# Kernel optimization log

Hardware: AMD Instinct MI355X
Metric: run time of the kernel (lower is better)

## Reference

```python
import jax, jax.numpy as jnp
import numpy as np

K = 16  # number of neighbors (module init arg)

def setup_inputs() -> dict:
    key = jax.random.key(0)
    M, D, N = 65536, 16, 64
    x = jax.random.normal(key, (M, D), dtype=jnp.float32)
    # equal-length segments: each point set has M // N points
    segs = jnp.full((N,), M // N, dtype=jnp.int64)
    return {"x": x, "segs": segs}

def reference(x, segs):
    # Segmented kNN graph. Segments are equal-length (static shapes for jit),
    # so the per-segment pairwise distance + top-k becomes a batched op.
    B = segs.shape[0]
    M, D = x.shape
    L = M // B  # points per segment
    pts = x.reshape(B, L, D)
    # squared euclidean distances within each segment: (B, L, L)
    sq = jnp.sum(pts * pts, axis=-1)
    d2 = sq[:, :, None] + sq[:, None, :] - 2.0 * jnp.einsum('bld,bmd->blm', pts, pts)
    # k smallest distances per point (includes self, as in DGL's knn_graph)
    _, idx = jax.lax.top_k(-d2, K)  # idx: (B, L, K), local indices within segment
    offsets = (jnp.arange(B, dtype=idx.dtype) * L)[:, None, None]
    src = (idx + offsets).reshape(-1)                      # neighbor -> global node id
    dst = (jnp.arange(L, dtype=idx.dtype)[None, :, None] + offsets)  # (B, L, 1)
    dst = jnp.broadcast_to(dst, (B, L, K)).reshape(-1)
    # edges point from k-nearest neighbors (predecessors) to each node
    return src, dst
```

## Files before the change

### kernel.cpp

```cpp
#include <hip/hip_runtime.h>
#include <stdint.h>


#define L_SEG 1024
#define M_PTS 65536

typedef __fp16 fp16x2 __attribute__((ext_vector_type(2)));
typedef __fp16 fp16x4 __attribute__((ext_vector_type(4)));
typedef float  f32x4  __attribute__((ext_vector_type(4)));

__device__ __forceinline__ uint32_t umn(uint32_t a, uint32_t b) { return a < b ? a : b; }
__device__ __forceinline__ uint32_t umx(uint32_t a, uint32_t b) { return a > b ? a : b; }

#define CE(arr, i, p) { uint32_t lo = umn(arr[i], arr[p]); uint32_t hi = umx(arr[i], arr[p]); arr[i] = lo; arr[p] = hi; }

__device__ __forceinline__ void clean16(uint32_t* A) {
    #pragma unroll
    for (int j = 8; j > 0; j >>= 1) {
        #pragma unroll
        for (int i = 0; i < 16; ++i) {
            int p = i ^ j;
            if (p > i) CE(A, i, p);
        }
    }
}

__device__ __forceinline__ void sort16(uint32_t* B) {
    #pragma unroll
    for (int p = 1; p < 16; p <<= 1) {
        #pragma unroll
        for (int k = p; k >= 1; k >>= 1) {
            #pragma unroll
            for (int j = (k & (p - 1)); j + k < 16; j += 2 * k) {
                #pragma unroll
                for (int i = 0; i <= ((k - 1 < 15 - j - k) ? k - 1 : 15 - j - k); ++i) {
                    if ((i + j) / (2 * p) == (i + j + k) / (2 * p)) CE(B, i + j, i + j + k);
                }
            }
        }
    }
}

__device__ __forceinline__ void keep16(uint32_t* A, const uint32_t* S) {
    #pragma unroll
    for (int i = 0; i < 16; ++i) A[i] = umn(A[i], S[15 - i]);
    clean16(A);
}

__device__ __forceinline__ void mergeg(uint32_t* A) {
    #pragma unroll
    for (int m = 16; m <= 32; m <<= 1) {
        uint32_t P[16];
        #pragma unroll
        for (int i = 0; i < 16; ++i) P[i] = (uint32_t)__shfl_xor((int)A[15 - i], m, 64);
        #pragma unroll
        for (int i = 0; i < 16; ++i) A[i] = umn(A[i], P[i]);
        clean16(A);
    }
}

__device__ __forceinline__ uint32_t sel4(const uint32_t* A, int g, int v) {
    uint32_t t01 = (g & 1) ? A[4 + v]  : A[v];
    uint32_t t23 = (g & 1) ? A[12 + v] : A[8 + v];
    return (g & 2) ? t23 : t01;
}

__global__ __launch_bounds__(256, 4) void knn_v9_kernel(const float* __restrict__ x,
                                                        int* __restrict__ out) {
    __shared__ __attribute__((aligned(16))) __fp16 sc[L_SEG * 16];
    __shared__ __attribute__((aligned(16))) float  ssq[L_SEG];
    __shared__ __attribute__((aligned(16))) __fp16 sq16[64 * 16];

    const int tid = threadIdx.x;
    const int b   = blockIdx.x;
    const int seg = (b & 7) * 8 + (b >> 7);
    const int qp  = (b >> 3) & 15;
    const float* xseg = x + (size_t)seg * (L_SEG * 16);
    const f32x4* gx4  = (const f32x4*)xseg;

    {
        fp16x4* scv = (fp16x4*)sc;
        #pragma unroll
        for (int i = 0; i < 16; ++i) {
            f32x4 v = gx4[tid + 256 * i];
            union { fp16x2 h2[2]; fp16x4 h4; } u;
            u.h2[0] = __builtin_amdgcn_cvt_pkrtz(-2.0f * v[0], -2.0f * v[1]);
            u.h2[1] = __builtin_amdgcn_cvt_pkrtz(-2.0f * v[2], -2.0f * v[3]);
            scv[tid + 256 * i] = u.h4;
        }
    }
    {
        const int c0 = tid << 2;
        #pragma unroll
        for (int c = 0; c < 4; ++c) {
            float s = 128.0f;
            #pragma unroll
            for (int d = 0; d < 4; ++d) {
                f32x4 v = gx4[(c0 + c) * 4 + d];
                s = __builtin_fmaf(v[0], v[0], s);
                s = __builtin_fmaf(v[1], v[1], s);
                s = __builtin_fmaf(v[2], v[2], s);
                s = __builtin_fmaf(v[3], v[3], s);
            }
            ssq[c0 + c] = s;
        }
    }
    if (tid < 64) {
        const f32x4* qg = gx4 + (size_t)(qp * 64 + tid) * 4;
        fp16x4* dst = (fp16x4*)(sq16 + (size_t)tid * 16);
        #pragma unroll
        for (int d = 0; d < 4; ++d) {
            f32x4 v = qg[d];
            union { fp16x2 h2[2]; fp16x4 h4; } u;
            u.h2[0] = __builtin_amdgcn_cvt_pkrtz(v[0], v[1]);
            u.h2[1] = __builtin_amdgcn_cvt_pkrtz(v[2], v[3]);
            dst[d] = u.h4;
        }
    }
    __syncthreads();

    const int lane = tid & 63;
    const int w    = tid >> 6;
    const int g    = lane >> 4;
    const int col  = lane & 15;
    const int qloc = qp * 64 + w * 16 + col;

    const fp16x4 bfrag = *(const fp16x4*)(sq16 + (size_t)(w * 16 + col) * 16 + g * 4);

    uint32_t A[16];
    #pragma unroll
    for (int i = 0; i < 16; ++i) A[i] = 0xFFFFFFFFu;

    const __fp16* ap  = sc + (size_t)col * 16 + g * 4;
    const float*  sqp = ssq + g * 4;
    const uint32_t vg4 = (uint32_t)(g << 2);

    #pragma unroll 2
    for (int it = 0; it < 4; ++it) {
        uint32_t P[16];
        #pragma unroll
        for (int t = 0; t < 16; ++t) {
            const int cb = it * 256 + t * 16;
            fp16x4 af = *(const fp16x4*)(ap + (size_t)cb * 16);
            f32x4  sq = *(const f32x4*)(sqp + cb);
            f32x4 acc = __builtin_amdgcn_mfma_f32_16x16x16f16(af, bfrag, sq, 0, 0, 0);
            const uint32_t ib = (uint32_t)cb + vg4;
            uint32_t k0 = (__float_as_uint(acc[0]) & 0xFFFFFC00u) | ib;
            uint32_t k1 = (__float_as_uint(acc[1]) & 0xFFFFFC00u) | (ib + 1u);
            uint32_t k2 = (__float_as_uint(acc[2]) & 0xFFFFFC00u) | (ib + 2u);
            uint32_t k3 = (__float_as_uint(acc[3]) & 0xFFFFFC00u) | (ib + 3u);
            P[t] = umn(umn(k0, k1), umn(k2, k3));
        }
        sort16(P);
        keep16(A, P);
    }

    mergeg(A);

    union H8 { f32x4 v[2]; fp16x2 h2[8]; };
    H8 qq;
    {
        const f32x4* qf = (const f32x4*)(sq16 + (size_t)(w * 16 + col) * 16);
        qq.v[0] = qf[0]; qq.v[1] = qf[1];
    }
    uint32_t R[16];
    #pragma unroll
    for (int v = 0; v < 4; ++v) {
        const uint32_t win = sel4(A, g, v);
        const uint32_t wi  = win & 1023u;
        const uint32_t qb  = wi & ~3u;
        const uint32_t wo  = wi & 3u;
        #pragma unroll
        for (int k = 0; k < 3; ++k) {
            const uint32_t o    = (uint32_t)k + (((uint32_t)k >= wo) ? 1u : 0u);
            const uint32_t pidx = qb + o;
            H8 cc;
            const f32x4* cf = (const f32x4*)(sc + (size_t)pidx * 16);
            cc.v[0] = cf[0]; cc.v[1] = cf[1];
            float s = 0.0f;
            #pragma unroll
            for (int j = 0; j < 8; ++j) {
#if __has_builtin(__builtin_amdgcn_fdot2)
                s = __builtin_amdgcn_fdot2(cc.h2[j], qq.h2[j], s, false);
#else
                s = __builtin_fmaf((float)cc.h2[j][0], (float)qq.h2[j][0], s);
                s = __builtin_fmaf((float)cc.h2[j][1], (float)qq.h2[j][1], s);
#endif
            }
            const float val = s + ssq[pidx];
            R[v * 3 + k] = (__float_as_uint(val) & 0xFFFFFC00u) | pidx;
        }
    }
    #pragma unroll
    for (int i = 12; i < 16; ++i) R[i] = 0xFFFFFFFFu;
    sort16(R);
    mergeg(R);
    keep16(A, R);

    const int base = seg * L_SEG;
    const int q    = base + qloc;
    int4 sv;
    sv.x = base + (int)(sel4(A, g, 0) & 1023u);
    sv.y = base + (int)(sel4(A, g, 1) & 1023u);
    sv.z = base + (int)(sel4(A, g, 2) & 1023u);
    sv.w = base + (int)(sel4(A, g, 3) & 1023u);
    ((int4*)out)[(size_t)q * 4 + g] = sv;
    ((int4*)out)[(size_t)M_PTS * 4 + (size_t)q * 4 + g] = make_int4(q, q, q, q);
}

extern "C" void kernel_launch(void* const* d_in, const int* in_sizes, int n_in,
                              void* d_out, int out_size, void* d_ws, size_t ws_size,
                              hipStream_t stream) {
    const float* x = (const float*)d_in[0];
    int* out = (int*)d_out;
    (void)d_ws; (void)ws_size;
    knn_v9_kernel<<<dim3(1024), dim3(256), 0, stream>>>(x, out);
}
```

Baseline: 86.45 us.

## Split candidate scan across two wave halves and merge top-k through shared memory

```diff
diff --git a/kernel.cpp b/kernel.cpp
--- a/kernel.cpp
+++ b/kernel.cpp
@@ -65,11 +65,12 @@
     return (g & 2) ? t23 : t01;
 }
 
-__global__ __launch_bounds__(256, 4) void knn_v9_kernel(const float* __restrict__ x,
-                                                        int* __restrict__ out) {
-    __shared__ __attribute__((aligned(16))) __fp16 sc[L_SEG * 16];
-    __shared__ __attribute__((aligned(16))) float  ssq[L_SEG];
-    __shared__ __attribute__((aligned(16))) __fp16 sq16[64 * 16];
+__global__ __launch_bounds__(512, 6) void knn_v10_kernel(const float* __restrict__ x,
+                                                         int* __restrict__ out) {
+    __shared__ __attribute__((aligned(16))) __fp16   sc[L_SEG * 16];
+    __shared__ __attribute__((aligned(16))) float    ssq[L_SEG];
+    __shared__ __attribute__((aligned(16))) __fp16   sq16[64 * 16];
+    __shared__ __attribute__((aligned(16))) uint32_t smerge[64][17];
 
     const int tid = threadIdx.x;
     const int b   = blockIdx.x;
@@ -81,18 +82,18 @@
     {
         fp16x4* scv = (fp16x4*)sc;
         #pragma unroll
-        for (int i = 0; i < 16; ++i) {
-            f32x4 v = gx4[tid + 256 * i];
+        for (int i = 0; i < 8; ++i) {
+            f32x4 v = gx4[tid + 512 * i];
             union { fp16x2 h2[2]; fp16x4 h4; } u;
             u.h2[0] = __builtin_amdgcn_cvt_pkrtz(-2.0f * v[0], -2.0f * v[1]);
             u.h2[1] = __builtin_amdgcn_cvt_pkrtz(-2.0f * v[2], -2.0f * v[3]);
-            scv[tid + 256 * i] = u.h4;
-        }
-    }
-    {
-        const int c0 = tid << 2;
-        #pragma unroll
-        for (int c = 0; c < 4; ++c) {
+            scv[tid + 512 * i] = u.h4;
+        }
+    }
+    {
+        const int c0 = tid << 1;
+        #pragma unroll
+        for (int c = 0; c < 2; ++c) {
             float s = 128.0f;
             #pragma unroll
             for (int d = 0; d < 4; ++d) {
@@ -121,26 +122,27 @@
 
     const int lane = tid & 63;
     const int w    = tid >> 6;
+    const int qg   = w & 3;
+    const int half = w >> 2;
     const int g    = lane >> 4;
     const int col  = lane & 15;
-    const int qloc = qp * 64 + w * 16 + col;
-
-    const fp16x4 bfrag = *(const fp16x4*)(sq16 + (size_t)(w * 16 + col) * 16 + g * 4);
-
-    uint32_t A[16];
-    #pragma unroll
-    for (int i = 0; i < 16; ++i) A[i] = 0xFFFFFFFFu;
+    const int qloc = qp * 64 + qg * 16 + col;
+
+    const fp16x4 bfrag = *(const fp16x4*)(sq16 + (size_t)(qg * 16 + col) * 16 + g * 4);
 
     const __fp16* ap  = sc + (size_t)col * 16 + g * 4;
     const float*  sqp = ssq + g * 4;
     const uint32_t vg4 = (uint32_t)(g << 2);
-
-    #pragma unroll 2
-    for (int it = 0; it < 4; ++it) {
-        uint32_t P[16];
+    const int hb = half * 512;
+
+    uint32_t A[16], P[16];
+    #pragma unroll
+    for (int it = 0; it < 2; ++it) {
+        uint32_t* D = it ? P : A;
+        const int cb0 = hb + it * 256;
         #pragma unroll
         for (int t = 0; t < 16; ++t) {
-            const int cb = it * 256 + t * 16;
+            const int cb = cb0 + t * 16;
             fp16x4 af = *(const fp16x4*)(ap + (size_t)cb * 16);
             f32x4  sq = *(const f32x4*)(sqp + cb);
             f32x4 acc = __builtin_amdgcn_mfma_f32_16x16x16f16(af, bfrag, sq, 0, 0, 0);
@@ -149,18 +151,33 @@
             uint32_t k1 = (__float_as_uint(acc[1]) & 0xFFFFFC00u) | (ib + 1u);
             uint32_t k2 = (__float_as_uint(acc[2]) & 0xFFFFFC00u) | (ib + 2u);
             uint32_t k3 = (__float_as_uint(acc[3]) & 0xFFFFFC00u) | (ib + 3u);
-            P[t] = umn(umn(k0, k1), umn(k2, k3));
-        }
-        sort16(P);
-        keep16(A, P);
-    }
+            D[t] = umn(umn(k0, k1), umn(k2, k3));
+        }
+        sort16(D);
+    }
+    keep16(A, P);
 
     mergeg(A);
+
+    const int qb = qg * 16 + col;
+    if (half == 1) {
+        #pragma unroll
+        for (int v = 0; v < 4; ++v) smerge[qb][g * 4 + v] = A[g * 4 + v];
+    }
+    __syncthreads();
+    if (half == 1) return;
+
+    {
+        uint32_t Q[16];
+        #pragma unroll
+        for (int i = 0; i < 16; ++i) Q[i] = smerge[qb][i];
+        keep16(A, Q);
+    }
 
     union H8 { f32x4 v[2]; fp16x2 h2[8]; };
     H8 qq;
     {
-        const f32x4* qf = (const f32x4*)(sq16 + (size_t)(w * 16 + col) * 16);
+        const f32x4* qf = (const f32x4*)(sq16 + (size_t)(qg * 16 + col) * 16);
         qq.v[0] = qf[0]; qq.v[1] = qf[1];
     }
     uint32_t R[16];
@@ -168,12 +185,12 @@
     for (int v = 0; v < 4; ++v) {
         const uint32_t win = sel4(A, g, v);
         const uint32_t wi  = win & 1023u;
-        const uint32_t qb  = wi & ~3u;
+        const uint32_t qbse = wi & ~3u;
         const uint32_t wo  = wi & 3u;
         #pragma unroll
         for (int k = 0; k < 3; ++k) {
             const uint32_t o    = (uint32_t)k + (((uint32_t)k >= wo) ? 1u : 0u);
-            const uint32_t pidx = qb + o;
+            const uint32_t pidx = qbse + o;
             H8 cc;
             const f32x4* cf = (const f32x4*)(sc + (size_t)pidx * 16);
             cc.v[0] = cf[0]; cc.v[1] = cf[1];
@@ -214,5 +231,5 @@
     const float* x = (const float*)d_in[0];
     int* out = (int*)d_out;
     (void)d_ws; (void)ws_size;
-    knn_v9_kernel<<<dim3(1024), dim3(256), 0, stream>>>(x, out);
-}
+    knn_v10_kernel<<<dim3(1024), dim3(512), 0, stream>>>(x, out);
+}
```

Result: no change. 86.53 us (+0.1%).

## Use FP8 MFMA for candidate scan, split candidates across waves, refine in fp32

Applied to the files above, without the earlier changes.

```diff
diff --git a/kernel.cpp b/kernel.cpp
--- a/kernel.cpp
+++ b/kernel.cpp
@@ -5,9 +5,14 @@
 #define L_SEG 1024
 #define M_PTS 65536
 
-typedef __fp16 fp16x2 __attribute__((ext_vector_type(2)));
-typedef __fp16 fp16x4 __attribute__((ext_vector_type(4)));
-typedef float  f32x4  __attribute__((ext_vector_type(4)));
+typedef float f32x4 __attribute__((ext_vector_type(4)));
+
+#define SC_OFF     0
+#define SSQ_OFF    16384
+#define SQF8_OFF   20480
+#define ZOFF       20992
+#define SMERGE_OFF 21008
+#define LDS_BYTES  23056
 
 __device__ __forceinline__ uint32_t umn(uint32_t a, uint32_t b) { return a < b ? a : b; }
 __device__ __forceinline__ uint32_t umx(uint32_t a, uint32_t b) { return a > b ? a : b; }
@@ -65,29 +70,25 @@
     return (g & 2) ? t23 : t01;
 }
 
-__global__ __launch_bounds__(256, 4) void knn_v9_kernel(const float* __restrict__ x,
-                                                        int* __restrict__ out) {
-    __shared__ __attribute__((aligned(16))) __fp16 sc[L_SEG * 16];
-    __shared__ __attribute__((aligned(16))) float  ssq[L_SEG];
-    __shared__ __attribute__((aligned(16))) __fp16 sq16[64 * 16];
-
-    const int tid = threadIdx.x;
-    const int b   = blockIdx.x;
-    const int seg = (b & 7) * 8 + (b >> 7);
-    const int qp  = (b >> 3) & 15;
+__global__ __launch_bounds__(256, 7) void knn_v11_kernel(const float* __restrict__ x,
+                                                         int* __restrict__ out) {
+    __shared__ __attribute__((aligned(16))) char smem[LDS_BYTES];
+
+    const int tid   = threadIdx.x;
+    const int b     = blockIdx.x;
+    const int seg   = (b & 7) * 8 + (b >> 8);
+    const int panel = (b >> 3) & 31;
+    const int qbase = panel * 32;
     const float* xseg = x + (size_t)seg * (L_SEG * 16);
     const f32x4* gx4  = (const f32x4*)xseg;
 
-    {
-        fp16x4* scv = (fp16x4*)sc;
-        #pragma unroll
-        for (int i = 0; i < 16; ++i) {
-            f32x4 v = gx4[tid + 256 * i];
-            union { fp16x2 h2[2]; fp16x4 h4; } u;
-            u.h2[0] = __builtin_amdgcn_cvt_pkrtz(-2.0f * v[0], -2.0f * v[1]);
-            u.h2[1] = __builtin_amdgcn_cvt_pkrtz(-2.0f * v[2], -2.0f * v[3]);
-            scv[tid + 256 * i] = u.h4;
-        }
+    #pragma unroll
+    for (int i = 0; i < 16; ++i) {
+        const int idx = tid + 256 * i;
+        f32x4 v = gx4[idx];
+        int lo = __builtin_amdgcn_cvt_pk_fp8_f32(-2.0f * v[0], -2.0f * v[1], 0, false);
+        int fl = __builtin_amdgcn_cvt_pk_fp8_f32(-2.0f * v[2], -2.0f * v[3], lo, true);
+        *(int*)(smem + SC_OFF + (size_t)idx * 4) = fl;
     }
     {
         const int c0 = tid << 2;
@@ -102,49 +103,60 @@
                 s = __builtin_fmaf(v[2], v[2], s);
                 s = __builtin_fmaf(v[3], v[3], s);
             }
-            ssq[c0 + c] = s;
-        }
-    }
-    if (tid < 64) {
-        const f32x4* qg = gx4 + (size_t)(qp * 64 + tid) * 4;
-        fp16x4* dst = (fp16x4*)(sq16 + (size_t)tid * 16);
+            ((float*)(smem + SSQ_OFF))[c0 + c] = s;
+        }
+    }
+    if (tid < 32) {
+        const f32x4* qr = gx4 + (size_t)(qbase + tid) * 4;
         #pragma unroll
         for (int d = 0; d < 4; ++d) {
-            f32x4 v = qg[d];
-            union { fp16x2 h2[2]; fp16x4 h4; } u;
-            u.h2[0] = __builtin_amdgcn_cvt_pkrtz(v[0], v[1]);
-            u.h2[1] = __builtin_amdgcn_cvt_pkrtz(v[2], v[3]);
-            dst[d] = u.h4;
-        }
-    }
+            f32x4 v = qr[d];
+            int lo = __builtin_amdgcn_cvt_pk_fp8_f32(v[0], v[1], 0, false);
+            int fl = __builtin_amdgcn_cvt_pk_fp8_f32(v[2], v[3], lo, true);
+            *(int*)(smem + SQF8_OFF + (size_t)tid * 16 + d * 4) = fl;
+        }
+    }
+    if (tid < 4) *(int*)(smem + ZOFF + tid * 4) = 0;
     __syncthreads();
 
-    const int lane = tid & 63;
-    const int w    = tid >> 6;
-    const int g    = lane >> 4;
-    const int col  = lane & 15;
-    const int qloc = qp * 64 + w * 16 + col;
-
-    const fp16x4 bfrag = *(const fp16x4*)(sq16 + (size_t)(w * 16 + col) * 16 + g * 4);
+    const int lane  = tid & 63;
+    const int w     = tid >> 6;
+    const int qg    = w & 1;
+    const int half  = w >> 1;
+    const int g     = lane >> 4;
+    const int col   = lane & 15;
+    const int qloc  = qg * 16 + col;
+    const int qglob = seg * L_SEG + qbase + qloc;
+
+    const char* baddr = (g < 2) ? (smem + SQF8_OFF + (size_t)qloc * 16 + g * 8)
+                                : (smem + ZOFF);
+    const long bfrag = *(const long*)baddr;
+
+    const char* abase = (g < 2) ? (smem + SC_OFF + (size_t)col * 16 + g * 8)
+                                : (smem + ZOFF);
+    const int   astep = (g < 2) ? 256 : 0;
 
     uint32_t A[16];
     #pragma unroll
     for (int i = 0; i < 16; ++i) A[i] = 0xFFFFFFFFu;
 
-    const __fp16* ap  = sc + (size_t)col * 16 + g * 4;
-    const float*  sqp = ssq + g * 4;
+    const float* ssq = (const float*)(smem + SSQ_OFF);
     const uint32_t vg4 = (uint32_t)(g << 2);
-
-    #pragma unroll 2
-    for (int it = 0; it < 4; ++it) {
+    const int hb = half * 512;
+    const char* aptr = abase + (size_t)hb * 16 * (astep ? 1 : 0);
+
+    #pragma unroll
+    for (int chain = 0; chain < 2; ++chain) {
         uint32_t P[16];
+        const int cb0 = hb + chain * 256;
         #pragma unroll
         for (int t = 0; t < 16; ++t) {
-            const int cb = it * 256 + t * 16;
-            fp16x4 af = *(const fp16x4*)(ap + (size_t)cb * 16);
-            f32x4  sq = *(const f32x4*)(sqp + cb);
-            f32x4 acc = __builtin_amdgcn_mfma_f32_16x16x16f16(af, bfrag, sq, 0, 0, 0);
-            const uint32_t ib = (uint32_t)cb + vg4;
+            const int tb = cb0 + t * 16;
+            const long a = *(const long*)aptr;
+            aptr += astep;
+            const f32x4 sq = *(const f32x4*)(ssq + tb + g * 4);
+            f32x4 acc = __builtin_amdgcn_mfma_f32_16x16x32_fp8_fp8(a, bfrag, sq, 0, 0, 0);
+            const uint32_t ib = (uint32_t)tb + vg4;
             uint32_t k0 = (__float_as_uint(acc[0]) & 0xFFFFFC00u) | ib;
             uint32_t k1 = (__float_as_uint(acc[1]) & 0xFFFFFC00u) | (ib + 1u);
             uint32_t k2 = (__float_as_uint(acc[2]) & 0xFFFFFC00u) | (ib + 2u);
@@ -157,37 +169,48 @@
 
     mergeg(A);
 
-    union H8 { f32x4 v[2]; fp16x2 h2[8]; };
-    H8 qq;
+    uint32_t* sm = (uint32_t*)(smem + SMERGE_OFF);
+    if (half == 1) {
+        #pragma unroll
+        for (int v = 0; v < 4; ++v) sm[qloc * 16 + g * 4 + v] = A[g * 4 + v];
+    }
+    __syncthreads();
+    if (half == 1) return;
     {
-        const f32x4* qf = (const f32x4*)(sq16 + (size_t)(w * 16 + col) * 16);
-        qq.v[0] = qf[0]; qq.v[1] = qf[1];
+        uint32_t Q[16];
+        #pragma unroll
+        for (int i = 0; i < 16; ++i) Q[i] = sm[qloc * 16 + i];
+        keep16(A, Q);
+    }
+
+    f32x4 qf[4];
+    {
+        const f32x4* qr = gx4 + (size_t)(qbase + qloc) * 4;
+        #pragma unroll
+        for (int d = 0; d < 4; ++d) qf[d] = qr[d];
     }
     uint32_t R[16];
     #pragma unroll
     for (int v = 0; v < 4; ++v) {
         const uint32_t win = sel4(A, g, v);
         const uint32_t wi  = win & 1023u;
-        const uint32_t qb  = wi & ~3u;
+        const uint32_t qb2 = wi & ~3u;
         const uint32_t wo  = wi & 3u;
         #pragma unroll
         for (int k = 0; k < 3; ++k) {
             const uint32_t o    = (uint32_t)k + (((uint32_t)k >= wo) ? 1u : 0u);
-            const uint32_t pidx = qb + o;
-            H8 cc;
-            const f32x4* cf = (const f32x4*)(sc + (size_t)pidx * 16);
-            cc.v[0] = cf[0]; cc.v[1] = cf[1];
+            const uint32_t pidx = qb2 + o;
+            const f32x4* cr = gx4 + (size_t)pidx * 4;
             float s = 0.0f;
             #pragma unroll
-            for (int j = 0; j < 8; ++j) {
-#if __has_builtin(__builtin_amdgcn_fdot2)
-                s = __builtin_amdgcn_fdot2(cc.h2[j], qq.h2[j], s, false);
-#else
-                s = __builtin_fmaf((float)cc.h2[j][0], (float)qq.h2[j][0], s);
-                s = __builtin_fmaf((float)cc.h2[j][1], (float)qq.h2[j][1], s);
-#endif
+            for (int d = 0; d < 4; ++d) {
+                f32x4 cv = cr[d];
+                s = __builtin_fmaf(cv[0], qf[d][0], s);
+                s = __builtin_fmaf(cv[1], qf[d][1], s);
+                s = __builtin_fmaf(cv[2], qf[d][2], s);
+                s = __builtin_fmaf(cv[3], qf[d][3], s);
             }
-            const float val = s + ssq[pidx];
+            const float val = __builtin_fmaf(s, -2.0f, ssq[pidx]);
             R[v * 3 + k] = (__float_as_uint(val) & 0xFFFFFC00u) | pidx;
         }
     }
@@ -198,7 +221,7 @@
     keep16(A, R);
 
     const int base = seg * L_SEG;
-    const int q    = base + qloc;
+    const int q    = qglob;
     int4 sv;
     sv.x = base + (int)(sel4(A, g, 0) & 1023u);
     sv.y = base + (int)(sel4(A, g, 1) & 1023u);
@@ -214,5 +237,5 @@
     const float* x = (const float*)d_in[0];
     int* out = (int*)d_out;
     (void)d_ws; (void)ws_size;
-    knn_v9_kernel<<<dim3(1024), dim3(256), 0, stream>>>(x, out);
-}
+    knn_v11_kernel<<<dim3(2048), dim3(256), 0, stream>>>(x, out);
+}
```

After: 115.6 us. 33.7% more time.
